# Kernel optimization log

Hardware: AMD Instinct MI355X
Metric: run time of the kernel (lower is better)

Reference implementation:

```python
import jax, jax.numpy as jnp
import numpy as np

DIM = 2048
NUM_HEADS = 16
HEAD_DIM = DIM // NUM_HEADS
BATCH, SEQ = 2, 2048


def setup_inputs() -> dict:
    key = jax.random.key(0)
    kx, kq, kk, kv, ko = jax.random.split(key, 5)
    scale = 1.0 / np.sqrt(DIM)
    return {
        "x": jax.random.normal(kx, (BATCH, SEQ, DIM), dtype=jnp.float32),
        "Wq": jax.random.normal(kq, (DIM, DIM), dtype=jnp.float32) * scale,
        "Wk": jax.random.normal(kk, (DIM, DIM), dtype=jnp.float32) * scale,
        "Wv": jax.random.normal(kv, (DIM, DIM), dtype=jnp.float32) * scale,
        "Wo": jax.random.normal(ko, (DIM, DIM), dtype=jnp.float32) * scale,
    }


def reference(x, Wq, Wk, Wv, Wo):
    b, s, _ = x.shape
    # QKV projections (flax Dense, no bias): y = x @ W
    q = (x @ Wq).reshape(b, s, NUM_HEADS, HEAD_DIM)
    k = (x @ Wk).reshape(b, s, NUM_HEADS, HEAD_DIM)
    v = (x @ Wv).reshape(b, s, NUM_HEADS, HEAD_DIM)
    # full (non-causal) softmax attention, scores are [b, h, q, k]
    scores = jnp.einsum('bqhd,bkhd->bhqk', q, k) * (HEAD_DIM ** -0.5)
    attn = jax.nn.softmax(scores, axis=-1)
    out = jnp.einsum('bhqk,bkhd->bqhd', attn, v).reshape(b, s, DIM)
    return out @ Wo
```

## Files before the change

kernel.cpp:

```cpp
#include <hip/hip_runtime.h>
#include <stdint.h>


typedef unsigned short u16;
typedef __attribute__((ext_vector_type(8))) short bf16x8;
typedef __attribute__((ext_vector_type(4))) float f32x4;

__device__ __forceinline__ u16 f2bf(float f) {
  union { float f; uint32_t u; } v; v.f = f;
  return (u16)((v.u + 0x7fffu + ((v.u >> 16) & 1u)) >> 16);
}

__device__ __forceinline__ float fast_exp2(float x) {
#if __has_builtin(__builtin_amdgcn_exp2f)
  return __builtin_amdgcn_exp2f(x);
#else
  return exp2f(x);
#endif
}

__device__ __forceinline__ void gl_lds16(const void* g, void* l) {
  __builtin_amdgcn_global_load_lds(
      (const __attribute__((address_space(1))) unsigned int*)g,
      (__attribute__((address_space(3))) unsigned int*)l, 16, 0, 0);
}

__global__ __launch_bounds__(256) void sniff_k(const u16* __restrict__ x,
                                               int* __restrict__ flag) {
  __shared__ int cnt;
  const int t = threadIdx.x;
  if (t == 0) cnt = 0;
  __syncthreads();
  int sane = 0;
#pragma unroll
  for (int i = 0; i < 16; ++i) {
    u16 u = x[t * 16 + i];
    int e = (u >> 7) & 0xff;
    sane += (e >= 90 && e <= 150) ? 1 : 0;
  }
  atomicAdd(&cnt, sane);
  __syncthreads();
  if (t == 0) *flag = (cnt >= 3700) ? 0 : 1;
}

__global__ __launch_bounds__(256) void convert_x_k(const void* __restrict__ xin,
                                                   u16* __restrict__ xb,
                                                   const int* __restrict__ flag) {
  if (*flag == 0) return;
  const int i = (blockIdx.x * 256 + threadIdx.x) * 8;
  const float* xf = (const float*)xin;
  float4 a = *(const float4*)(xf + i);
  float4 b = *(const float4*)(xf + i + 4);
  bf16x8 o;
  o[0] = (short)f2bf(a.x); o[1] = (short)f2bf(a.y);
  o[2] = (short)f2bf(a.z); o[3] = (short)f2bf(a.w);
  o[4] = (short)f2bf(b.x); o[5] = (short)f2bf(b.y);
  o[6] = (short)f2bf(b.z); o[7] = (short)f2bf(b.w);
  *(bf16x8*)(xb + i) = o;
}

__global__ __launch_bounds__(256) void convert_transpose_k(const void* __restrict__ w0,
                                                           const void* __restrict__ w1,
                                                           const void* __restrict__ w2,
                                                           const void* __restrict__ w3,
                                                           u16* __restrict__ out_base,
                                                           const int* __restrict__ flag) {
  __shared__ u16 tile[64][66];
  const int z = blockIdx.z;
  const void* in = (z == 0) ? w0 : (z == 1) ? w1 : (z == 2) ? w2 : w3;
  u16* out = out_base + (size_t)z * 4194304u;
  const int tr = blockIdx.y, tc = blockIdx.x, t = threadIdx.x;
  if (*flag) {
    const float* inf32 = (const float*)in;
#pragma unroll
    for (int i = 0; i < 16; ++i) {
      int idx = t + i * 256, r = idx >> 6, c = idx & 63;
      tile[r][c] = f2bf(inf32[(size_t)(tr * 64 + r) * 2048 + tc * 64 + c]);
    }
  } else {
    const u16* inb = (const u16*)in;
#pragma unroll
    for (int i = 0; i < 16; ++i) {
      int idx = t + i * 256, r = idx >> 6, c = idx & 63;
      tile[r][c] = inb[(size_t)(tr * 64 + r) * 2048 + tc * 64 + c];
    }
  }
  __syncthreads();
#pragma unroll
  for (int i = 0; i < 16; ++i) {
    int idx = t + i * 256, r = idx >> 6, c = idx & 63;
    out[(size_t)(tc * 64 + r) * 2048 + tr * 64 + c] = tile[c][r];
  }
}

__global__ __launch_bounds__(256) void transpose_k(const u16* __restrict__ in,
                                                   u16* __restrict__ out) {
  __shared__ u16 tile[64][66];
  const size_t zoff = (size_t)blockIdx.z * 4194304u;
  in += zoff; out += zoff;
  const int tr = blockIdx.y, tc = blockIdx.x, t = threadIdx.x;
#pragma unroll
  for (int i = 0; i < 16; ++i) {
    int idx = t + i * 256, r = idx >> 6, c = idx & 63;
    tile[r][c] = in[(size_t)(tr * 64 + r) * 2048 + tc * 64 + c];
  }
  __syncthreads();
#pragma unroll
  for (int i = 0; i < 16; ++i) {
    int idx = t + i * 256, r = idx >> 6, c = idx & 63;
    out[(size_t)(tc * 64 + r) * 2048 + tr * 64 + c] = tile[c][r];
  }
}

__global__ __launch_bounds__(256) void gemm_bt(const u16* __restrict__ A,
                                               const void* __restrict__ Araw,
                                               const int* __restrict__ aflag,
                                               const u16* __restrict__ Bt,
                                               u16* __restrict__ C0,
                                               u16* __restrict__ C1,
                                               u16* __restrict__ C2,
                                               float qscale,
                                               const int* __restrict__ outflag) {
  __shared__ u16 As[128 * 64];
  __shared__ u16 Bs[128 * 64];
  const int bx = blockIdx.x, by = blockIdx.y, t = threadIdx.x;
  const int wave = t >> 6, lane = t & 63;
  const int g = lane >> 4, lq = lane & 15;
  const int wr = wave >> 1, wc = wave & 1;
  const int which = bx >> 4, nb = bx & 15;
  u16* C = (which == 0) ? C0 : ((which == 1) ? C1 : C2);
  const float scale = (which == 0) ? qscale : 1.0f;
  const u16* Ause = (aflag && *aflag == 0) ? (const u16*)Araw : A;
  const int lr = lane >> 3, lcs = ((lane & 7) ^ lr) * 8;

  const u16* Arow = Ause + (size_t)(by * 128) * 2048;
  const u16* Brow = Bt + (size_t)(bx * 128) * 2048;

  int cofs[2];
#pragma unroll
  for (int ks = 0; ks < 2; ++ks) cofs[ks] = ((ks * 4 + g) ^ (lq & 7)) * 8;

  f32x4 acc[4][4];
#pragma unroll
  for (int i = 0; i < 4; ++i)
#pragma unroll
    for (int j = 0; j < 4; ++j) acc[i][j] = f32x4{0.f, 0.f, 0.f, 0.f};

  for (int kb = 0; kb < 2048; kb += 64) {
    __syncthreads();
#pragma unroll
    for (int i = 0; i < 4; ++i) {
      const int r = wave * 32 + i * 8;
      gl_lds16(Arow + (size_t)(r + lr) * 2048 + kb + lcs, &As[r * 64]);
      gl_lds16(Brow + (size_t)(r + lr) * 2048 + kb + lcs, &Bs[r * 64]);
    }
    __syncthreads();
#pragma unroll
    for (int ks = 0; ks < 2; ++ks) {
      bf16x8 af[4], bfr[4];
#pragma unroll
      for (int mt = 0; mt < 4; ++mt)
        af[mt] = *(const bf16x8*)(&As[(wr * 64 + mt * 16 + lq) * 64 + cofs[ks]]);
#pragma unroll
      for (int nt = 0; nt < 4; ++nt)
        bfr[nt] = *(const bf16x8*)(&Bs[(wc * 64 + nt * 16 + lq) * 64 + cofs[ks]]);
#pragma unroll
      for (int mt = 0; mt < 4; ++mt)
#pragma unroll
        for (int nt = 0; nt < 4; ++nt)
          acc[mt][nt] = __builtin_amdgcn_mfma_f32_16x16x32_bf16(af[mt], bfr[nt], acc[mt][nt], 0, 0, 0);
    }
  }
  const int outF32 = outflag ? *outflag : 0;
#pragma unroll
  for (int mt = 0; mt < 4; ++mt)
#pragma unroll
    for (int nt = 0; nt < 4; ++nt)
#pragma unroll
      for (int j = 0; j < 4; ++j) {
        size_t row = (size_t)(by * 128 + wr * 64 + mt * 16 + g * 4 + j);
        size_t col = (size_t)(nb * 128 + wc * 64 + nt * 16 + lq);
        float v = acc[mt][nt][j] * scale;
        if (outF32) ((float*)C)[row * 2048 + col] = v;
        else C[row * 2048 + col] = f2bf(v);
      }
}

__global__ __launch_bounds__(256) void attn_kernel(const u16* __restrict__ Q,
                                                   const u16* __restrict__ K,
                                                   const u16* __restrict__ Vt,
                                                   u16* __restrict__ O) {
  __shared__ u16 Ks[64 * 128];
  __shared__ u16 Vs[128 * 64];
  __shared__ u16 Ps[4][16][72];

  const int qb = blockIdx.x, h = blockIdx.y, b = blockIdx.z;
  const int t = threadIdx.x, wave = t >> 6, lane = t & 63;
  const int g = lane >> 4, lq = lane & 15;

  const size_t qk_base = ((size_t)b * 2048) * 2048 + (size_t)h * 128;
  const size_t vt_base = ((size_t)b * 2048 + (size_t)h * 128) * 2048;

  bf16x8 qf[4];
  {
    const u16* qp = Q + qk_base + (size_t)(qb * 64 + wave * 16 + lq) * 2048 + g * 8;
#pragma unroll
    for (int kk = 0; kk < 4; ++kk) qf[kk] = *(const bf16x8*)(qp + kk * 32);
  }

  f32x4 acc_o[8];
#pragma unroll
  for (int i = 0; i < 8; ++i) acc_o[i] = f32x4{0.f, 0.f, 0.f, 0.f};
  float l_run = 0.f;

  const int vlr = lane >> 3, vlcs = ((lane & 7) ^ vlr) * 8;

  int kofs[4];
#pragma unroll
  for (int kk = 0; kk < 4; ++kk) kofs[kk] = ((kk * 4 + g) ^ (lq & 7)) * 8;

  for (int kb = 0; kb < 2048; kb += 64) {
    __syncthreads();
#pragma unroll
    for (int i = 0; i < 4; ++i) {
      const int win = wave * 2 + (i >> 1), half = i & 1;
      const int kr = half * 4 + (lane >> 4);
      const int kc = (lane & 15) ^ kr;
      gl_lds16(K + qk_base + (size_t)(kb + win * 8 + kr) * 2048 + kc * 8,
               &Ks[win * 1024 + half * 512]);
      const int vr = wave * 32 + i * 8;
      gl_lds16(Vt + vt_base + (size_t)(vr + vlr) * 2048 + kb + vlcs,
               &Vs[vr * 64]);
    }
    __syncthreads();

    f32x4 st[4];
#pragma unroll
    for (int mt = 0; mt < 4; ++mt) st[mt] = f32x4{0.f, 0.f, 0.f, 0.f};
#pragma unroll
    for (int kk = 0; kk < 4; ++kk)
#pragma unroll
      for (int mt = 0; mt < 4; ++mt) {
        bf16x8 af = *(const bf16x8*)(&Ks[(mt * 16 + lq) * 128 + kofs[kk]]);
        st[mt] = __builtin_amdgcn_mfma_f32_16x16x32_bf16(af, qf[kk], st[mt], 0, 0, 0);
      }

#pragma unroll
    for (int mt = 0; mt < 4; ++mt) {
      uint32_t u[4];
#pragma unroll
      for (int j = 0; j < 4; ++j) {
        float p = fast_exp2(st[mt][j]);
        u[j] = __float_as_uint(p) & 0xffff0000u;
        l_run += __uint_as_float(u[j]);
      }
      uint2 pk;
      pk.x = (u[0] >> 16) | u[1];
      pk.y = (u[2] >> 16) | u[3];
      *(uint2*)(&Ps[wave][lq][mt * 16 + g * 4]) = pk;
    }

#pragma unroll
    for (int kk = 0; kk < 2; ++kk) {
      bf16x8 af = *(const bf16x8*)(&Ps[wave][lq][kk * 32 + g * 8]);
#pragma unroll
      for (int nt = 0; nt < 8; ++nt) {
        bf16x8 bfr = *(const bf16x8*)(&Vs[(nt * 16 + lq) * 64 + ((kk * 4 + g) ^ (lq & 7)) * 8]);
        acc_o[nt] = __builtin_amdgcn_mfma_f32_16x16x32_bf16(af, bfr, acc_o[nt], 0, 0, 0);
      }
    }
  }

  l_run += __shfl_xor(l_run, 16);
  l_run += __shfl_xor(l_run, 32);
  const float i0 = 1.f / __shfl(l_run, g * 4 + 0);
  const float i1 = 1.f / __shfl(l_run, g * 4 + 1);
  const float i2 = 1.f / __shfl(l_run, g * 4 + 2);
  const float i3 = 1.f / __shfl(l_run, g * 4 + 3);
  u16* op = O + ((size_t)b * 2048 + qb * 64 + wave * 16) * 2048 + h * 128;
#pragma unroll
  for (int nt = 0; nt < 8; ++nt) {
    op[(size_t)(g * 4 + 0) * 2048 + nt * 16 + lq] = f2bf(acc_o[nt][0] * i0);
    op[(size_t)(g * 4 + 1) * 2048 + nt * 16 + lq] = f2bf(acc_o[nt][1] * i1);
    op[(size_t)(g * 4 + 2) * 2048 + nt * 16 + lq] = f2bf(acc_o[nt][2] * i2);
    op[(size_t)(g * 4 + 3) * 2048 + nt * 16 + lq] = f2bf(acc_o[nt][3] * i3);
  }
}

extern "C" void kernel_launch(void* const* d_in, const int* in_sizes, int n_in,
                              void* d_out, int out_size, void* d_ws, size_t ws_size,
                              hipStream_t stream) {
  const void* x  = d_in[0];
  const void* Wq = d_in[1];
  const void* Wk = d_in[2];
  const void* Wv = d_in[3];
  const void* Wo = d_in[4];
  u16* ws = (u16*)d_ws;

  const size_t SLOT = 4194304u;
  u16* xb  = ws + 0 * SLOT;
  u16* WqT = ws + 2 * SLOT;
  u16* WoT = ws + 5 * SLOT;
  u16* Qb  = ws + 6 * SLOT;
  u16* Kb  = ws + 8 * SLOT;
  u16* Vb  = ws + 10 * SLOT;
  int* flag = (int*)(ws + 12 * SLOT);
  u16* VTd = (u16*)d_out;
  u16* Ab  = Qb;

  sniff_k<<<1, 256, 0, stream>>>((const u16*)x, flag);

  convert_x_k<<<4096, 256, 0, stream>>>(x, xb, flag);
  convert_transpose_k<<<dim3(32, 32, 4), 256, 0, stream>>>(Wq, Wk, Wv, Wo, WqT, flag);

  const float QSCALE = 0.12751745f;
  gemm_bt<<<dim3(48, 32), 256, 0, stream>>>(xb, x, flag, WqT, Qb, Kb, Vb,
                                            QSCALE, nullptr);

  transpose_k<<<dim3(32, 32, 2), 256, 0, stream>>>(Vb, VTd);

  attn_kernel<<<dim3(32, 16, 2), dim3(256), 0, stream>>>(Qb, Kb, VTd, Ab);

  gemm_bt<<<dim3(16, 32), 256, 0, stream>>>(Ab, Ab, nullptr, WoT,
                                            (u16*)d_out, (u16*)d_out, (u16*)d_out,
                                            1.0f, flag);
}
```

Baseline: 454.9 us.

## Process two query tiles per attention block and compute row sums via MFMA

Each attention block now handles 128 query rows (two 64-row halves), so every K/V tile loaded into LDS is reused twice, halving global K/V traffic and the grid size. The softmax denominator is now an extra MFMA against a row of bf16 ones stored in LDS, replacing per-element scalar adds and cross-lane shuffles. This raises register pressure (two output accumulator sets) and halves the block count to 512, which may reduce occupancy.

```diff
diff --git a/kernel.cpp b/kernel.cpp
--- a/kernel.cpp
+++ b/kernel.cpp
@@ -191,8 +191,8 @@
                                                    const u16* __restrict__ Vt,
                                                    u16* __restrict__ O) {
   __shared__ u16 Ks[64 * 128];
-  __shared__ u16 Vs[128 * 64];
-  __shared__ u16 Ps[4][16][72];
+  __shared__ u16 Vs[144 * 64];
+  __shared__ u16 Ps[4][2][16][72];
 
   const int qb = blockIdx.x, h = blockIdx.y, b = blockIdx.z;
   const int t = threadIdx.x, wave = t >> 6, lane = t & 63;
@@ -201,20 +201,27 @@
   const size_t qk_base = ((size_t)b * 2048) * 2048 + (size_t)h * 128;
   const size_t vt_base = ((size_t)b * 2048 + (size_t)h * 128) * 2048;
 
-  bf16x8 qf[4];
-  {
-    const u16* qp = Q + qk_base + (size_t)(qb * 64 + wave * 16 + lq) * 2048 + g * 8;
-#pragma unroll
-    for (int kk = 0; kk < 4; ++kk) qf[kk] = *(const bf16x8*)(qp + kk * 32);
-  }
-
-  f32x4 acc_o[8];
-#pragma unroll
-  for (int i = 0; i < 8; ++i) acc_o[i] = f32x4{0.f, 0.f, 0.f, 0.f};
-  float l_run = 0.f;
+  *(__attribute__((ext_vector_type(4))) short*)(&Vs[128 * 64 + t * 4]) =
+      (__attribute__((ext_vector_type(4))) short){0x3f80, 0x3f80, 0x3f80, 0x3f80};
+
+  bf16x8 qf[2][4];
+#pragma unroll
+  for (int qh = 0; qh < 2; ++qh) {
+    const u16* qp = Q + qk_base +
+                    (size_t)(qb * 128 + qh * 64 + wave * 16 + lq) * 2048 + g * 8;
+#pragma unroll
+    for (int kk = 0; kk < 4; ++kk) qf[qh][kk] = *(const bf16x8*)(qp + kk * 32);
+  }
+
+  f32x4 acc_o[2][8], acc_l[2];
+#pragma unroll
+  for (int qh = 0; qh < 2; ++qh) {
+    acc_l[qh] = f32x4{0.f, 0.f, 0.f, 0.f};
+#pragma unroll
+    for (int i = 0; i < 8; ++i) acc_o[qh][i] = f32x4{0.f, 0.f, 0.f, 0.f};
+  }
 
   const int vlr = lane >> 3, vlcs = ((lane & 7) ^ vlr) * 8;
-
   int kofs[4];
 #pragma unroll
   for (int kk = 0; kk < 4; ++kk) kofs[kk] = ((kk * 4 + g) ^ (lq & 7)) * 8;
@@ -234,56 +241,59 @@
     }
     __syncthreads();
 
-    f32x4 st[4];
-#pragma unroll
-    for (int mt = 0; mt < 4; ++mt) st[mt] = f32x4{0.f, 0.f, 0.f, 0.f};
-#pragma unroll
-    for (int kk = 0; kk < 4; ++kk)
+#pragma unroll
+    for (int qh = 0; qh < 2; ++qh) {
+      f32x4 st[4];
+#pragma unroll
+      for (int mt = 0; mt < 4; ++mt) st[mt] = f32x4{0.f, 0.f, 0.f, 0.f};
+#pragma unroll
+      for (int kk = 0; kk < 4; ++kk)
+#pragma unroll
+        for (int mt = 0; mt < 4; ++mt) {
+          bf16x8 af = *(const bf16x8*)(&Ks[(mt * 16 + lq) * 128 + kofs[kk]]);
+          st[mt] = __builtin_amdgcn_mfma_f32_16x16x32_bf16(af, qf[qh][kk], st[mt], 0, 0, 0);
+        }
+
 #pragma unroll
       for (int mt = 0; mt < 4; ++mt) {
-        bf16x8 af = *(const bf16x8*)(&Ks[(mt * 16 + lq) * 128 + kofs[kk]]);
-        st[mt] = __builtin_amdgcn_mfma_f32_16x16x32_bf16(af, qf[kk], st[mt], 0, 0, 0);
+        uint32_t u0 = __float_as_uint(fast_exp2(st[mt][0]));
+        uint32_t u1 = __float_as_uint(fast_exp2(st[mt][1]));
+        uint32_t u2 = __float_as_uint(fast_exp2(st[mt][2]));
+        uint32_t u3 = __float_as_uint(fast_exp2(st[mt][3]));
+        uint2 pk;
+        pk.x = (u0 >> 16) | (u1 & 0xffff0000u);
+        pk.y = (u2 >> 16) | (u3 & 0xffff0000u);
+        *(uint2*)(&Ps[wave][qh][lq][mt * 16 + g * 4]) = pk;
       }
 
 #pragma unroll
-    for (int mt = 0; mt < 4; ++mt) {
-      uint32_t u[4];
-#pragma unroll
-      for (int j = 0; j < 4; ++j) {
-        float p = fast_exp2(st[mt][j]);
-        u[j] = __float_as_uint(p) & 0xffff0000u;
-        l_run += __uint_as_float(u[j]);
+      for (int kk = 0; kk < 2; ++kk) {
+        bf16x8 af = *(const bf16x8*)(&Ps[wave][qh][lq][kk * 32 + g * 8]);
+#pragma unroll
+        for (int nt = 0; nt < 8; ++nt) {
+          bf16x8 bfr = *(const bf16x8*)(&Vs[(nt * 16 + lq) * 64 + ((kk * 4 + g) ^ (lq & 7)) * 8]);
+          acc_o[qh][nt] = __builtin_amdgcn_mfma_f32_16x16x32_bf16(af, bfr, acc_o[qh][nt], 0, 0, 0);
+        }
+        bf16x8 ones = *(const bf16x8*)(&Vs[(128 + lq) * 64 + ((kk * 4 + g) ^ (lq & 7)) * 8]);
+        acc_l[qh] = __builtin_amdgcn_mfma_f32_16x16x32_bf16(af, ones, acc_l[qh], 0, 0, 0);
       }
-      uint2 pk;
-      pk.x = (u[0] >> 16) | u[1];
-      pk.y = (u[2] >> 16) | u[3];
-      *(uint2*)(&Ps[wave][lq][mt * 16 + g * 4]) = pk;
-    }
-
-#pragma unroll
-    for (int kk = 0; kk < 2; ++kk) {
-      bf16x8 af = *(const bf16x8*)(&Ps[wave][lq][kk * 32 + g * 8]);
-#pragma unroll
-      for (int nt = 0; nt < 8; ++nt) {
-        bf16x8 bfr = *(const bf16x8*)(&Vs[(nt * 16 + lq) * 64 + ((kk * 4 + g) ^ (lq & 7)) * 8]);
-        acc_o[nt] = __builtin_amdgcn_mfma_f32_16x16x32_bf16(af, bfr, acc_o[nt], 0, 0, 0);
-      }
-    }
-  }
-
-  l_run += __shfl_xor(l_run, 16);
-  l_run += __shfl_xor(l_run, 32);
-  const float i0 = 1.f / __shfl(l_run, g * 4 + 0);
-  const float i1 = 1.f / __shfl(l_run, g * 4 + 1);
-  const float i2 = 1.f / __shfl(l_run, g * 4 + 2);
-  const float i3 = 1.f / __shfl(l_run, g * 4 + 3);
-  u16* op = O + ((size_t)b * 2048 + qb * 64 + wave * 16) * 2048 + h * 128;
-#pragma unroll
-  for (int nt = 0; nt < 8; ++nt) {
-    op[(size_t)(g * 4 + 0) * 2048 + nt * 16 + lq] = f2bf(acc_o[nt][0] * i0);
-    op[(size_t)(g * 4 + 1) * 2048 + nt * 16 + lq] = f2bf(acc_o[nt][1] * i1);
-    op[(size_t)(g * 4 + 2) * 2048 + nt * 16 + lq] = f2bf(acc_o[nt][2] * i2);
-    op[(size_t)(g * 4 + 3) * 2048 + nt * 16 + lq] = f2bf(acc_o[nt][3] * i3);
+    }
+  }
+
+#pragma unroll
+  for (int qh = 0; qh < 2; ++qh) {
+    const float i0 = 1.f / acc_l[qh][0];
+    const float i1 = 1.f / acc_l[qh][1];
+    const float i2 = 1.f / acc_l[qh][2];
+    const float i3 = 1.f / acc_l[qh][3];
+    u16* op = O + ((size_t)b * 2048 + qb * 128 + qh * 64 + wave * 16) * 2048 + h * 128;
+#pragma unroll
+    for (int nt = 0; nt < 8; ++nt) {
+      op[(size_t)(g * 4 + 0) * 2048 + nt * 16 + lq] = f2bf(acc_o[qh][nt][0] * i0);
+      op[(size_t)(g * 4 + 1) * 2048 + nt * 16 + lq] = f2bf(acc_o[qh][nt][1] * i1);
+      op[(size_t)(g * 4 + 2) * 2048 + nt * 16 + lq] = f2bf(acc_o[qh][nt][2] * i2);
+      op[(size_t)(g * 4 + 3) * 2048 + nt * 16 + lq] = f2bf(acc_o[qh][nt][3] * i3);
+    }
   }
 }
 
@@ -319,7 +329,7 @@
 
   transpose_k<<<dim3(32, 32, 2), 256, 0, stream>>>(Vb, VTd);
 
-  attn_kernel<<<dim3(32, 16, 2), dim3(256), 0, stream>>>(Qb, Kb, VTd, Ab);
+  attn_kernel<<<dim3(16, 16, 2), dim3(256), 0, stream>>>(Qb, Kb, VTd, Ab);
 
   gemm_bt<<<dim3(16, 32), 256, 0, stream>>>(Ab, Ab, nullptr, WoT,
                                             (u16*)d_out, (u16*)d_out, (u16*)d_out,
```

After: 457.0 us. Within noise of the previous version (+0.5%).
